# Kernel optimization log

Hardware: AMD Instinct MI355X
Metric: run time of the kernel (lower is better)

## Reference

```python
import jax, jax.numpy as jnp
import numpy as np
import math

B, T, E, H, L, FF = 8, 512, 1024, 16, 4, 4096
D = E // H
LN_EPS = 1e-5


def _layernorm(x, g, b):
    mu = jnp.mean(x, axis=-1, keepdims=True)
    var = jnp.mean((x - mu) ** 2, axis=-1, keepdims=True)
    return (x - mu) * jax.lax.rsqrt(var + LN_EPS) * g + b


def setup_inputs() -> dict:
    key = jax.random.key(0)
    ks = jax.random.split(key, 16)
    s = 0.02
    return {
        "src": jax.random.normal(ks[0], (B, T, E), jnp.float32),
        "in_proj_w": jax.random.normal(ks[1], (L, 3 * E, E), jnp.float32) * s,
        "in_proj_b": jax.random.normal(ks[2], (L, 3 * E), jnp.float32) * s,
        "out_w": jax.random.normal(ks[3], (L, E, E), jnp.float32) * s,
        "out_b": jnp.zeros((L, E), jnp.float32),
        "ff1_w": jax.random.normal(ks[4], (L, FF, E), jnp.float32) * s,
        "ff1_b": jnp.zeros((L, FF), jnp.float32),
        "ff2_w": jax.random.normal(ks[5], (L, E, FF), jnp.float32) * s,
        "ff2_b": jnp.zeros((L, E), jnp.float32),
        "ln1_g": jnp.ones((L, E), jnp.float32),
        "ln1_b": jnp.zeros((L, E), jnp.float32),
        "ln2_g": jnp.ones((L, E), jnp.float32),
        "ln2_b": jnp.zeros((L, E), jnp.float32),
        "head_w": jax.random.normal(ks[6], (1, E), jnp.float32) * s,
        "head_b": jnp.zeros((1,), jnp.float32),
    }


def reference(src, in_proj_w, in_proj_b, out_w, out_b, ff1_w, ff1_b,
              ff2_w, ff2_b, ln1_g, ln1_b, ln2_g, ln2_b, head_w, head_b):
    b, t, e = src.shape
    # --- PositionalEncoding (faithful to batch_first bug: pe indexed by batch dim) ---
    pos = jnp.arange(b, dtype=jnp.float32)[:, None]            # [B,1]
    div = jnp.exp(jnp.arange(0, e, 2, dtype=jnp.float32) * (-math.log(10000.0) / e))
    pe = jnp.zeros((b, e), jnp.float32)
    pe = pe.at[:, 0::2].set(jnp.sin(pos * div)).at[:, 1::2].set(jnp.cos(pos * div))
    x = src + pe[:, None, :]                                   # broadcast over seq

    # --- Gaussian bias, shared across layers (Tq == Tk == T) ---
    dist = jnp.arange(t)[:, None] - jnp.arange(t)[None, :]
    gb = jnp.exp(-(dist.astype(jnp.float32) ** 2) / (2.0 * (t / 4.0) ** 2))  # [T,T]

    for l in range(L):
        qkv = x @ in_proj_w[l].T + in_proj_b[l]                # [B,T,3E]
        q, k, v = jnp.split(qkv, 3, axis=-1)
        q = q.reshape(b, t, H, D).transpose(0, 2, 1, 3)        # [B,H,T,D]
        k = k.reshape(b, t, H, D).transpose(0, 2, 1, 3)
        v = v.reshape(b, t, H, D).transpose(0, 2, 1, 3)
        scores = jnp.einsum("bhqd,bhkd->bhqk", q, k) / math.sqrt(D)
        w = jax.nn.softmax(scores, axis=-1)                    # [B,H,Tq,Tk]
        w = w * gb[None, None]
        w = w / (jnp.sum(w, axis=-1, keepdims=True) + 1e-5)
        o = jnp.einsum("bhqk,bhkd->bhqd", w, v)
        o = o.transpose(0, 2, 1, 3).reshape(b, t, e)
        o = o @ out_w[l].T + out_b[l]
        x = _layernorm(x + o, ln1_g[l], ln1_b[l])              # post-norm
        ff = jax.nn.relu(x @ ff1_w[l].T + ff1_b[l]) @ ff2_w[l].T + ff2_b[l]
        x = _layernorm(x + ff, ln2_g[l], ln2_b[l])

    last = x[:, -1, :]                                         # [B,E]
    return last @ head_w.T + head_b                            # [B,1]
```

## Files before the change

kernel.cpp:

```cpp
#include <hip/hip_runtime.h>

typedef unsigned short u16;
typedef __attribute__((ext_vector_type(4))) float v4f;
typedef __attribute__((ext_vector_type(8))) short v8bf;

__device__ inline u16 f2bf(float f){
  union { float f; unsigned u; } v; v.f = f;
  unsigned r = (v.u + 0x7FFFu + ((v.u >> 16) & 1u)) >> 16;
  return (u16)r;
}
__device__ inline float bf2f(u16 u){
  union { unsigned u; float f; } v; v.u = ((unsigned)u) << 16;
  return v.f;
}

#define GLD_LDS16(gp, lp) \
  __builtin_amdgcn_global_load_lds((const __attribute__((address_space(1))) void*)(gp), \
                                   (__attribute__((address_space(3))) void*)(lp), 16, 0, 0)
#define VMCNT(n) asm volatile("s_waitcnt vmcnt(" #n ")" ::: "memory")
#define LGKM0 do { asm volatile("s_waitcnt lgkmcnt(0)" ::: "memory"); \
                   __builtin_amdgcn_sched_barrier(0); } while (0)

template<int FUSE>
__global__ __launch_bounds__(512, 2) void gemm8(
    const u16* __restrict__ A, const u16* __restrict__ W,
    const float* __restrict__ bias, void* __restrict__ C,
    int N, int K, int Kc, int gx, int gy)
{
  __shared__ u16 smem[65536];
  const int tid = threadIdx.x, lane = tid & 63, wid = tid >> 6;
  const int wm = wid >> 2, wn = wid & 3;

  const int nwg = gridDim.x, bid = blockIdx.x;
  const int swz = (bid & 7) * (nwg >> 3) + (bid >> 3);
  const int gxy = gx * gy;
  const int bz = swz / gxy;
  const int rem = swz - bz * gxy;
  const int by = rem / gx;
  const int bx = rem - by * gx;
  const int k0 = bz * Kc;
  const int NT = Kc >> 6;

  const int arow = (wid >> 1) * 16 + (lane & 15);
  const int akk  = (wid & 1) * 32 + ((lane >> 4) << 3);
  const u16* gA = A + (size_t)(by * 256 + arow) * K + k0 + akk;
  const u16* gB = W + (size_t)(bx * 256 + arow) * K + k0 + akk;
  u16* ldst = smem + tid * 8;

  auto stageA = [&](int t, int h) {
    u16* d = ldst + (t & 1) * 32768 + h * 8192;
    const u16* s = gA + (size_t)(h * 128) * K + t * 64;
    GLD_LDS16(s, d);
    GLD_LDS16(s + (size_t)64 * K, d + 4096);
  };
  auto stageB = [&](int t, int h) {
    u16* d = ldst + (t & 1) * 32768 + (2 + h) * 8192;
    const u16* s = gB + (size_t)(h * 128) * K + t * 64;
    GLD_LDS16(s, d);
    GLD_LDS16(s + (size_t)64 * K, d + 4096);
  };

  v4f acc[8][4];
  #pragma unroll
  for (int i = 0; i < 8; ++i)
    #pragma unroll
    for (int j = 0; j < 4; ++j) acc[i][j] = (v4f){0.f, 0.f, 0.f, 0.f};

  stageA(0, 0); stageB(0, 0); stageB(0, 1); stageA(0, 1);
  if (NT > 1) { stageA(1, 0); stageA(1, 1); }
  if (NT > 2) { VMCNT(4); } else { VMCNT(0); }
  __builtin_amdgcn_s_barrier();

  const u16* rdA = smem + wm * 8192 + lane * 8;
  const u16* rdB = smem + 16384 + (wn >> 1) * 8192 + lane * 8;
  const int jb = (wn & 1) * 4;

  v8bf aq[4][2], bq[2][2];

#define PHASE(QI, QJ, LOADA, LOADB, STAGE_CODE, VM_CODE)                        \
  {                                                                             \
    const int bufo = (t & 1) * 32768;                                           \
    if (LOADA) {                                                                \
      _Pragma("unroll") for (int m = 0; m < 4; ++m)                             \
        _Pragma("unroll") for (int kk = 0; kk < 2; ++kk)                        \
          aq[m][kk] = *(const v8bf*)(rdA + bufo + (((QI)*4 + m)*2 + kk)*512);   \
    }                                                                           \
    if (LOADB) {                                                                \
      _Pragma("unroll") for (int n = 0; n < 2; ++n)                             \
        _Pragma("unroll") for (int kk = 0; kk < 2; ++kk)                        \
          bq[n][kk] = *(const v8bf*)(rdB + bufo + ((jb + (QJ)*2 + n)*2 + kk)*512);\
    }                                                                           \
    STAGE_CODE;                                                                 \
    VM_CODE;                                                                    \
    __builtin_amdgcn_s_barrier();                                               \
    LGKM0;                                                                      \
    __builtin_amdgcn_s_setprio(1);                                              \
    _Pragma("unroll") for (int m = 0; m < 4; ++m)                               \
      _Pragma("unroll") for (int n = 0; n < 2; ++n)                             \
        _Pragma("unroll") for (int kk = 0; kk < 2; ++kk)                        \
          acc[(QI)*4 + m][(QJ)*2 + n] = __builtin_amdgcn_mfma_f32_16x16x32_bf16(\
              aq[m][kk], bq[n][kk], acc[(QI)*4 + m][(QJ)*2 + n], 0, 0, 0);      \
    __builtin_amdgcn_s_setprio(0);                                              \
    __builtin_amdgcn_s_barrier();                                               \
  }

  for (int t = 0; t < NT; ++t) {
    PHASE(0, 0, true,  true,
          { if (t + 1 < NT) { stageB(t + 1, 0); stageB(t + 1, 1); } }, {});
    PHASE(0, 1, false, true,  {}, {});
    PHASE(1, 1, true,  false, {}, {});
    PHASE(1, 0, false, true,
          { if (t + 2 < NT) { stageA(t + 2, 0); stageA(t + 2, 1); } },
          { if (t == NT - 2) { VMCNT(0); } else if (t < NT - 2) { VMCNT(4); } });
  }
#undef PHASE

  const int cn0 = bx * 256 + wn * 64 + (lane & 15);
  const int rm0 = by * 256 + wm * 128 + ((lane >> 4) << 2);
  if (FUSE == 2) {
    u16* Cp = (u16*)C + (size_t)bz * 4096 * N;
    #pragma unroll
    for (int i = 0; i < 8; ++i)
      #pragma unroll
      for (int r = 0; r < 4; ++r) {
        size_t ro = (size_t)(rm0 + i * 16 + r) * N + cn0;
        #pragma unroll
        for (int j = 0; j < 4; ++j) Cp[ro + j * 16] = f2bf(acc[i][j][r]);
      }
  } else {
    float bv[4];
    #pragma unroll
    for (int j = 0; j < 4; ++j) bv[j] = bias[cn0 + j * 16];
    u16* Cp = (u16*)C;
    #pragma unroll
    for (int i = 0; i < 8; ++i)
      #pragma unroll
      for (int r = 0; r < 4; ++r) {
        size_t ro = (size_t)(rm0 + i * 16 + r) * N + cn0;
        #pragma unroll
        for (int j = 0; j < 4; ++j) {
          float v = acc[i][j][r] + bv[j];
          if (FUSE == 1) v = fmaxf(v, 0.f);
          Cp[ro + j * 16] = f2bf(v);
        }
      }
  }
}

__global__ __launch_bounds__(256, 2) void attn_f(const u16* __restrict__ qkv,
                                                 u16* __restrict__ o)
{
  __shared__ u16 Kf[2][4096];
  __shared__ u16 Vt[2][4096];
  __shared__ u16 wbuf[64 * 72];
  const int tid = threadIdx.x, lane = tid & 63, wid = tid >> 6;
  const int grp = lane >> 4, li = lane & 15;
  const int bh = blockIdx.y, b = bh >> 4, h = bh & 15;
  const int q0 = blockIdx.x * 64;
  const u16* Qg = qkv + (size_t)b * 512 * 3072 + h * 64;
  const u16* Kg = Qg + 1024;
  const u16* Vg = Qg + 2048;

  const size_t qrow = (size_t)(q0 + wid * 16 + li) * 3072;
  v8bf qa0 = *(const v8bf*)(Qg + qrow + grp * 8);
  v8bf qa1 = *(const v8bf*)(Qg + qrow + 32 + grp * 8);

  const u16* kga = Kg + (size_t)(wid * 16 + li) * 3072 + grp * 8;
  auto k_stage = [&](int kt, int buf) {
    #pragma unroll
    for (int s = 0; s < 2; ++s)
      GLD_LDS16(kga + (size_t)kt * 64 * 3072 + s * 32, &Kf[buf][(wid * 2 + s) * 512]);
  };
  auto v_load = [&](int kt, int x) -> v8bf {
    int u = x * 256 + tid, kk = u >> 3, d0 = (u & 7) * 8;
    return *(const v8bf*)(Vg + (size_t)(kt * 64 + kk) * 3072 + d0);
  };
  auto vt_write = [&](int buf, int x, v8bf v) {
    int u = x * 256 + tid, kk = u >> 3, d0 = (u & 7) * 8;
    int kg = (kk >> 3) & 3, kks = kk >> 5, jb2 = (kk & 7) * 2;
    #pragma unroll
    for (int i = 0; i < 8; ++i) {
      int d = d0 + i;
      int byte = (((d >> 4) * 2 + kks) * 1024 + ((d & 15) + 16 * kg) * 16 + jb2)
                 ^ (((d >> 4) & 3) << 5);
      *(u16*)((char*)&Vt[buf][0] + byte) = (u16)v[i];
    }
  };

  v4f oacc[4];
  #pragma unroll
  for (int nt = 0; nt < 4; ++nt) oacc[nt] = (v4f){0.f, 0.f, 0.f, 0.f};
  float mreg[4] = {-1e30f, -1e30f, -1e30f, -1e30f};
  float sg[4] = {0.f, 0.f, 0.f, 0.f};
  float fqv[4];
  #pragma unroll
  for (int j = 0; j < 4; ++j) fqv[j] = (float)(q0 + wid * 16 + grp * 4 + j);

  v8bf vst[2][2];
  k_stage(0, 0);
  k_stage(1, 1);
  vst[0][0] = v_load(0, 0); vst[0][1] = v_load(0, 1);
  VMCNT(0);
  vt_write(0, 0, vst[0][0]); vt_write(0, 1, vst[0][1]);
  vst[1][0] = v_load(1, 0); vst[1][1] = v_load(1, 1);
  LGKM0;
  __builtin_amdgcn_s_barrier();

  const float GC = 3.0517578125e-05f;

  #pragma unroll
  for (int t = 0; t < 8; ++t) {
    const int cur = t & 1;
    v8bf bq0[4], bq1[4];
    #pragma unroll
    for (int nb = 0; nb < 4; ++nb) {
      bq0[nb] = *(const v8bf*)&Kf[cur][(nb * 2 + 0) * 512 + lane * 8];
      bq1[nb] = *(const v8bf*)&Kf[cur][(nb * 2 + 1) * 512 + lane * 8];
    }
    v4f pa[4];
    #pragma unroll
    for (int nb = 0; nb < 4; ++nb) {
      v4f z = (v4f){0.f, 0.f, 0.f, 0.f};
      z = __builtin_amdgcn_mfma_f32_16x16x32_bf16(qa0, bq0[nb], z, 0, 0, 0);
      pa[nb] = __builtin_amdgcn_mfma_f32_16x16x32_bf16(qa1, bq1[nb], z, 0, 0, 0);
    }
    if (t < 7) {
      __builtin_amdgcn_s_barrier();
      __builtin_amdgcn_sched_barrier(0);
      if (t + 2 < 8) k_stage(t + 2, cur);
      if (t < 6) { VMCNT(2); } else { VMCNT(0); }
      vt_write((t + 1) & 1, 0, vst[(t + 1) & 1][0]);
      vt_write((t + 1) & 1, 1, vst[(t + 1) & 1][1]);
      if (t + 2 < 8) { vst[t & 1][0] = v_load(t + 2, 0); vst[t & 1][1] = v_load(t + 2, 1); }
    }
    #pragma unroll
    for (int nb = 0; nb < 4; ++nb) {
      const float fk = (float)(t * 64 + nb * 16 + li);
      #pragma unroll
      for (int j = 0; j < 4; ++j) {
        float d = fqv[j] - fk;
        pa[nb][j] = pa[nb][j] * 0.125f - d * d * GC;
      }
    }
    #pragma unroll
    for (int j = 0; j < 4; ++j) {
      float tmax = fmaxf(fmaxf(pa[0][j], pa[1][j]), fmaxf(pa[2][j], pa[3][j]));
      tmax = fmaxf(tmax, __shfl_xor(tmax, 1));
      tmax = fmaxf(tmax, __shfl_xor(tmax, 2));
      tmax = fmaxf(tmax, __shfl_xor(tmax, 4));
      tmax = fmaxf(tmax, __shfl_xor(tmax, 8));
      float mn = fmaxf(mreg[j], tmax);
      float sc = __expf(mreg[j] - mn);
      mreg[j] = mn;
      float rs = 0.f;
      #pragma unroll
      for (int nb = 0; nb < 4; ++nb) {
        float e = __expf(pa[nb][j] - mn);
        pa[nb][j] = e;
        rs += e;
      }
      rs += __shfl_xor(rs, 1); rs += __shfl_xor(rs, 2);
      rs += __shfl_xor(rs, 4); rs += __shfl_xor(rs, 8);
      sg[j] = sg[j] * sc + rs;
      #pragma unroll
      for (int nt = 0; nt < 4; ++nt) oacc[nt][j] *= sc;
    }
    #pragma unroll
    for (int j = 0; j < 4; ++j) {
      const int row = wid * 16 + grp * 4 + j;
      #pragma unroll
      for (int nb = 0; nb < 4; ++nb)
        wbuf[row * 72 + ((nb * 16 + li) ^ (grp << 3))] = f2bf(pa[nb][j]);
    }
    const int swr = ((li >> 2) & 3) << 3;
    v8bf af0 = *(const v8bf*)&wbuf[(wid * 16 + li) * 72 + ((0 * 32 + grp * 8) ^ swr)];
    v8bf af1 = *(const v8bf*)&wbuf[(wid * 16 + li) * 72 + ((1 * 32 + grp * 8) ^ swr)];
    #pragma unroll
    for (int nt = 0; nt < 4; ++nt) {
      v8bf bv0 = *(const v8bf*)((char*)&Vt[cur][0] + ((((nt * 2 + 0) * 1024) + lane * 16) ^ ((nt & 3) << 5)));
      v8bf bv1 = *(const v8bf*)((char*)&Vt[cur][0] + ((((nt * 2 + 1) * 1024) + lane * 16) ^ ((nt & 3) << 5)));
      oacc[nt] = __builtin_amdgcn_mfma_f32_16x16x32_bf16(af0, bv0, oacc[nt], 0, 0, 0);
      oacc[nt] = __builtin_amdgcn_mfma_f32_16x16x32_bf16(af1, bv1, oacc[nt], 0, 0, 0);
    }
    if (t < 7) {
      if (t < 6) { VMCNT(2); } else { VMCNT(0); }
      LGKM0;
      __builtin_amdgcn_s_barrier();
      __builtin_amdgcn_sched_barrier(0);
    }
  }

  float rin[4];
  #pragma unroll
  for (int j = 0; j < 4; ++j) rin[j] = 1.f / sg[j];
  const size_t obase = (size_t)(b * 512 + q0 + wid * 16 + grp * 4) * 1024 + h * 64;
  #pragma unroll
  for (int nt = 0; nt < 4; ++nt)
    #pragma unroll
    for (int j = 0; j < 4; ++j)
      o[obase + (size_t)j * 1024 + nt * 16 + li] = f2bf(oacc[nt][j] * rin[j]);
}

__global__ __launch_bounds__(256) void ln_res4_k(
    const float* __restrict__ x, const u16* __restrict__ part,
    const float* __restrict__ bias, const float* __restrict__ g,
    const float* __restrict__ beta, float* __restrict__ y, u16* __restrict__ yb)
{
  const int row = blockIdx.x, tid = threadIdx.x;
  const size_t base = (size_t)row * 1024 + tid * 4;
  const size_t MN = 4096ull * 1024;
  float4 xv = *(const float4*)(x + base);
  const int e = tid * 4;
  float4 bb = *(const float4*)(bias + e);
  float v0 = xv.x + bb.x, v1 = xv.y + bb.y, v2 = xv.z + bb.z, v3 = xv.w + bb.w;
  #pragma unroll
  for (int q = 0; q < 4; ++q) {
    ushort4 pv = *(const ushort4*)(part + q * MN + base);
    v0 += bf2f(pv.x); v1 += bf2f(pv.y); v2 += bf2f(pv.z); v3 += bf2f(pv.w);
  }
  float s = v0 + v1 + v2 + v3;
  float q2 = v0*v0 + v1*v1 + v2*v2 + v3*v3;
  #pragma unroll
  for (int m = 1; m < 64; m <<= 1) { s += __shfl_xor(s, m); q2 += __shfl_xor(q2, m); }
  __shared__ float ls[4], lq[4];
  if ((tid & 63) == 0) { ls[tid >> 6] = s; lq[tid >> 6] = q2; }
  __syncthreads();
  s = ls[0] + ls[1] + ls[2] + ls[3];
  q2 = lq[0] + lq[1] + lq[2] + lq[3];
  const float mu = s * (1.f / 1024.f);
  const float var = q2 * (1.f / 1024.f) - mu * mu;
  const float rs = rsqrtf(var + 1e-5f);
  float4 gv = *(const float4*)(g + e);
  float4 be = *(const float4*)(beta + e);
  float o0 = (v0 - mu) * rs * gv.x + be.x;
  float o1 = (v1 - mu) * rs * gv.y + be.y;
  float o2 = (v2 - mu) * rs * gv.z + be.z;
  float o3 = (v3 - mu) * rs * gv.w + be.w;
  *(float4*)(y + base) = make_float4(o0, o1, o2, o3);
  ushort4 ob; ob.x = f2bf(o0); ob.y = f2bf(o1); ob.z = f2bf(o2); ob.w = f2bf(o3);
  *(ushort4*)(yb + base) = ob;
}

__global__ __launch_bounds__(256) void pe_add_k(const float* __restrict__ src,
    float* __restrict__ xf, u16* __restrict__ xb)
{
  const int idx = blockIdx.x * 256 + threadIdx.x;
  const int e = idx & 1023;
  const int b = idx >> 19;
  float freq = __expf((float)(e >> 1) * (-18.420680743952367f * (1.f / 1024.f)));
  float ang = (float)b * freq;
  float pe = (e & 1) ? cosf(ang) : sinf(ang);
  float v = src[idx] + pe;
  xf[idx] = v;
  xb[idx] = f2bf(v);
}

__global__ __launch_bounds__(256) void cvt4_k(const float* __restrict__ s0,
    const float* __restrict__ s1, const float* __restrict__ s2,
    const float* __restrict__ s3, u16* __restrict__ dst)
{
  int i = blockIdx.x * 256 + threadIdx.x;
  const float* s; size_t off;
  if (i < 786432)       { s = s0; off = (size_t)i; }
  else if (i < 1048576) { s = s1; off = (size_t)i - 786432; }
  else if (i < 2097152) { s = s2; off = (size_t)i - 1048576; }
  else                  { s = s3; off = (size_t)i - 2097152; }
  float4 v = ((const float4*)s)[off];
  ushort4 ov; ov.x = f2bf(v.x); ov.y = f2bf(v.y); ov.z = f2bf(v.z); ov.w = f2bf(v.w);
  ((ushort4*)dst)[i] = ov;
}

__global__ __launch_bounds__(256) void head_k(const float* __restrict__ xf,
    const float* __restrict__ hw, const float* __restrict__ hb, float* __restrict__ out)
{
  const int b = blockIdx.x, tid = threadIdx.x;
  const float4 xv = ((const float4*)(xf + ((size_t)b * 512 + 511) * 1024))[tid];
  const float4 wv = ((const float4*)hw)[tid];
  float s = xv.x * wv.x + xv.y * wv.y + xv.z * wv.z + xv.w * wv.w;
  #pragma unroll
  for (int m = 1; m < 64; m <<= 1) s += __shfl_xor(s, m);
  __shared__ float ls[4];
  if ((tid & 63) == 0) ls[tid >> 6] = s;
  __syncthreads();
  if (tid == 0) out[b] = ls[0] + ls[1] + ls[2] + ls[3] + hb[0];
}

extern "C" void kernel_launch(void* const* d_in, const int* in_sizes, int n_in,
                              void* d_out, int out_size, void* d_ws, size_t ws_size,
                              hipStream_t stream)
{
  const float* src  = (const float*)d_in[0];
  const float* ipw  = (const float*)d_in[1];
  const float* ipb  = (const float*)d_in[2];
  const float* outw = (const float*)d_in[3];
  const float* outb = (const float*)d_in[4];
  const float* f1w  = (const float*)d_in[5];
  const float* f1b  = (const float*)d_in[6];
  const float* f2w  = (const float*)d_in[7];
  const float* f2b  = (const float*)d_in[8];
  const float* l1g  = (const float*)d_in[9];
  const float* l1b  = (const float*)d_in[10];
  const float* l2g  = (const float*)d_in[11];
  const float* l2b  = (const float*)d_in[12];
  const float* hw   = (const float*)d_in[13];
  const float* hb   = (const float*)d_in[14];

  char* p = (char*)d_ws;
  auto take = [&](size_t bytes) { char* r = p; p += (bytes + 255) & ~(size_t)255; return r; };
  float* xf   = (float*)take(4096ull * 1024 * 4);
  u16*   xb   = (u16*)  take(4096ull * 1024 * 2);
  u16*   slA  = (u16*)  take(4096ull * 4096 * 2);
  u16*   ob   = (u16*)  take(4096ull * 1024 * 2);
  u16*   pf   = (u16*)  take(4ull * 4096 * 1024 * 2);
  u16*   wc   = (u16*)  take(12582912ull * 2);

  u16* qkvb = slA;
  u16* f1o  = slA;

  pe_add_k<<<16384, 256, 0, stream>>>(src, xf, xb);

  for (int l = 0; l < 4; ++l) {
    cvt4_k<<<12288, 256, 0, stream>>>(ipw + (size_t)l * 3145728,
                                      outw + (size_t)l * 1048576,
                                      f1w + (size_t)l * 4194304,
                                      f2w + (size_t)l * 4194304, wc);
    gemm8<0><<<192, 512, 0, stream>>>(xb, wc, ipb + l * 3072, qkvb, 3072, 1024, 1024, 12, 16);
    attn_f<<<dim3(8, 128), 256, 0, stream>>>(qkvb, ob);
    gemm8<2><<<256, 512, 0, stream>>>(ob, wc + 3145728, nullptr, pf, 1024, 1024, 256, 4, 16);
    ln_res4_k<<<4096, 256, 0, stream>>>(xf, pf, outb + l * 1024, l1g + l * 1024, l1b + l * 1024, xf, xb);
    gemm8<1><<<256, 512, 0, stream>>>(xb, wc + 4194304, f1b + l * 4096, f1o, 4096, 1024, 1024, 16, 16);
    gemm8<2><<<256, 512, 0, stream>>>(f1o, wc + 8388608, nullptr, pf, 1024, 4096, 1024, 4, 16);
    ln_res4_k<<<4096, 256, 0, stream>>>(xf, pf, f2b + l * 1024, l2g + l * 1024, l2b + l * 1024, xf, xb);
  }
  head_k<<<8, 256, 0, stream>>>(xf, hw, hb, (float*)d_out);
}
```

Before: 910.8 us.

## Replace 256x256 double-buffered GEMM with 128x256 triple-buffered K=32 pipeline

Shrinks the GEMM output tile from 256x256 to 128x256 and the K step from 64 to 32, with a three-stage LDS ring buffer and one barrier per step instead of the four-phase schedule. LDS per block and accumulator registers drop, so launch bounds now request 4 blocks per CU, and the grids double to give more workgroups. The aim is more latency hiding and better CU fill. The cost is lower arithmetic intensity per tile, more A/B reloads from global memory, and more barriers per unit of compute.

New measurement: 1.032 ms. 13.3% more time.

```diff
diff --git a/kernel.cpp b/kernel.cpp
--- a/kernel.cpp
+++ b/kernel.cpp
@@ -22,12 +22,12 @@
                    __builtin_amdgcn_sched_barrier(0); } while (0)
 
 template<int FUSE>
-__global__ __launch_bounds__(512, 2) void gemm8(
+__global__ __launch_bounds__(512, 4) void gemm3(
     const u16* __restrict__ A, const u16* __restrict__ W,
     const float* __restrict__ bias, void* __restrict__ C,
     int N, int K, int Kc, int gx, int gy)
 {
-  __shared__ u16 smem[65536];
+  __shared__ u16 smem[36864];
   const int tid = threadIdx.x, lane = tid & 63, wid = tid >> 6;
   const int wm = wid >> 2, wn = wid & 3;
 
@@ -38,110 +38,84 @@
   const int rem = swz - bz * gxy;
   const int by = rem / gx;
   const int bx = rem - by * gx;
+  const int m0 = by * 128, n0 = bx * 256;
   const int k0 = bz * Kc;
-  const int NT = Kc >> 6;
-
-  const int arow = (wid >> 1) * 16 + (lane & 15);
-  const int akk  = (wid & 1) * 32 + ((lane >> 4) << 3);
-  const u16* gA = A + (size_t)(by * 256 + arow) * K + k0 + akk;
-  const u16* gB = W + (size_t)(bx * 256 + arow) * K + k0 + akk;
+  const int NT = Kc >> 5;
+
+  const int l15 = lane & 15, kc8 = (lane >> 4) * 8;
+  const u16* srcA  = A + (size_t)(m0 + wid * 16 + l15) * K + k0 + kc8;
+  const u16* srcB0 = W + (size_t)(n0 + wid * 16 + l15) * K + k0 + kc8;
+  const u16* srcB1 = W + (size_t)(n0 + 128 + wid * 16 + l15) * K + k0 + kc8;
   u16* ldst = smem + tid * 8;
 
-  auto stageA = [&](int t, int h) {
-    u16* d = ldst + (t & 1) * 32768 + h * 8192;
-    const u16* s = gA + (size_t)(h * 128) * K + t * 64;
-    GLD_LDS16(s, d);
-    GLD_LDS16(s + (size_t)64 * K, d + 4096);
+  auto stage = [&](int t) {
+    u16* d = ldst + (t % 3) * 12288;
+    const int ko = t * 32;
+    GLD_LDS16(srcA  + ko, d);
+    GLD_LDS16(srcB0 + ko, d + 4096);
+    GLD_LDS16(srcB1 + ko, d + 8192);
   };
-  auto stageB = [&](int t, int h) {
-    u16* d = ldst + (t & 1) * 32768 + (2 + h) * 8192;
-    const u16* s = gB + (size_t)(h * 128) * K + t * 64;
-    GLD_LDS16(s, d);
-    GLD_LDS16(s + (size_t)64 * K, d + 4096);
-  };
-
-  v4f acc[8][4];
-  #pragma unroll
-  for (int i = 0; i < 8; ++i)
-    #pragma unroll
-    for (int j = 0; j < 4; ++j) acc[i][j] = (v4f){0.f, 0.f, 0.f, 0.f};
-
-  stageA(0, 0); stageB(0, 0); stageB(0, 1); stageA(0, 1);
-  if (NT > 1) { stageA(1, 0); stageA(1, 1); }
-  if (NT > 2) { VMCNT(4); } else { VMCNT(0); }
+
+  v4f acc[4][4];
+  #pragma unroll
+  for (int m = 0; m < 4; ++m)
+    #pragma unroll
+    for (int n = 0; n < 4; ++n) acc[m][n] = (v4f){0.f, 0.f, 0.f, 0.f};
+
+  stage(0); stage(1);
+  VMCNT(3);
   __builtin_amdgcn_s_barrier();
 
-  const u16* rdA = smem + wm * 8192 + lane * 8;
-  const u16* rdB = smem + 16384 + (wn >> 1) * 8192 + lane * 8;
-  const int jb = (wn & 1) * 4;
-
-  v8bf aq[4][2], bq[2][2];
-
-#define PHASE(QI, QJ, LOADA, LOADB, STAGE_CODE, VM_CODE)                        \
-  {                                                                             \
-    const int bufo = (t & 1) * 32768;                                           \
-    if (LOADA) {                                                                \
-      _Pragma("unroll") for (int m = 0; m < 4; ++m)                             \
-        _Pragma("unroll") for (int kk = 0; kk < 2; ++kk)                        \
-          aq[m][kk] = *(const v8bf*)(rdA + bufo + (((QI)*4 + m)*2 + kk)*512);   \
-    }                                                                           \
-    if (LOADB) {                                                                \
-      _Pragma("unroll") for (int n = 0; n < 2; ++n)                             \
-        _Pragma("unroll") for (int kk = 0; kk < 2; ++kk)                        \
-          bq[n][kk] = *(const v8bf*)(rdB + bufo + ((jb + (QJ)*2 + n)*2 + kk)*512);\
-    }                                                                           \
-    STAGE_CODE;                                                                 \
-    VM_CODE;                                                                    \
-    __builtin_amdgcn_s_barrier();                                               \
-    LGKM0;                                                                      \
-    __builtin_amdgcn_s_setprio(1);                                              \
-    _Pragma("unroll") for (int m = 0; m < 4; ++m)                               \
-      _Pragma("unroll") for (int n = 0; n < 2; ++n)                             \
-        _Pragma("unroll") for (int kk = 0; kk < 2; ++kk)                        \
-          acc[(QI)*4 + m][(QJ)*2 + n] = __builtin_amdgcn_mfma_f32_16x16x32_bf16(\
-              aq[m][kk], bq[n][kk], acc[(QI)*4 + m][(QJ)*2 + n], 0, 0, 0);      \
-    __builtin_amdgcn_s_setprio(0);                                              \
-    __builtin_amdgcn_s_barrier();                                               \
+  const u16* rdA = smem + (wm * 4) * 512 + lane * 8;
+  const u16* rdB = smem + 4096 + (wn * 4) * 512 + lane * 8;
+
+  for (int t = 0; t < NT; ++t) {
+    const int bo = (t % 3) * 12288;
+    v8bf aq[4], bq[4];
+    #pragma unroll
+    for (int m = 0; m < 4; ++m) aq[m] = *(const v8bf*)(rdA + bo + m * 512);
+    #pragma unroll
+    for (int n = 0; n < 4; ++n) bq[n] = *(const v8bf*)(rdB + bo + n * 512);
+    if (t + 2 < NT) stage(t + 2);
+    LGKM0;
+    __builtin_amdgcn_s_setprio(1);
+    #pragma unroll
+    for (int m = 0; m < 4; ++m)
+      #pragma unroll
+      for (int n = 0; n < 4; ++n)
+        acc[m][n] = __builtin_amdgcn_mfma_f32_16x16x32_bf16(aq[m], bq[n], acc[m][n], 0, 0, 0);
+    __builtin_amdgcn_s_setprio(0);
+    if (t < NT - 2) { VMCNT(3); } else if (t == NT - 2) { VMCNT(0); }
+    __builtin_amdgcn_s_barrier();
   }
 
-  for (int t = 0; t < NT; ++t) {
-    PHASE(0, 0, true,  true,
-          { if (t + 1 < NT) { stageB(t + 1, 0); stageB(t + 1, 1); } }, {});
-    PHASE(0, 1, false, true,  {}, {});
-    PHASE(1, 1, true,  false, {}, {});
-    PHASE(1, 0, false, true,
-          { if (t + 2 < NT) { stageA(t + 2, 0); stageA(t + 2, 1); } },
-          { if (t == NT - 2) { VMCNT(0); } else if (t < NT - 2) { VMCNT(4); } });
-  }
-#undef PHASE
-
-  const int cn0 = bx * 256 + wn * 64 + (lane & 15);
-  const int rm0 = by * 256 + wm * 128 + ((lane >> 4) << 2);
+  const int cn0 = n0 + wn * 64 + l15;
+  const int rm0 = m0 + wm * 64 + ((lane >> 4) << 2);
   if (FUSE == 2) {
     u16* Cp = (u16*)C + (size_t)bz * 4096 * N;
     #pragma unroll
-    for (int i = 0; i < 8; ++i)
+    for (int m = 0; m < 4; ++m)
       #pragma unroll
       for (int r = 0; r < 4; ++r) {
-        size_t ro = (size_t)(rm0 + i * 16 + r) * N + cn0;
+        size_t ro = (size_t)(rm0 + m * 16 + r) * N + cn0;
         #pragma unroll
-        for (int j = 0; j < 4; ++j) Cp[ro + j * 16] = f2bf(acc[i][j][r]);
+        for (int n = 0; n < 4; ++n) Cp[ro + n * 16] = f2bf(acc[m][n][r]);
       }
   } else {
     float bv[4];
     #pragma unroll
-    for (int j = 0; j < 4; ++j) bv[j] = bias[cn0 + j * 16];
+    for (int n = 0; n < 4; ++n) bv[n] = bias[cn0 + n * 16];
     u16* Cp = (u16*)C;
     #pragma unroll
-    for (int i = 0; i < 8; ++i)
+    for (int m = 0; m < 4; ++m)
       #pragma unroll
       for (int r = 0; r < 4; ++r) {
-        size_t ro = (size_t)(rm0 + i * 16 + r) * N + cn0;
+        size_t ro = (size_t)(rm0 + m * 16 + r) * N + cn0;
         #pragma unroll
-        for (int j = 0; j < 4; ++j) {
-          float v = acc[i][j][r] + bv[j];
+        for (int n = 0; n < 4; ++n) {
+          float v = acc[m][n][r] + bv[n];
           if (FUSE == 1) v = fmaxf(v, 0.f);
-          Cp[ro + j * 16] = f2bf(v);
+          Cp[ro + n * 16] = f2bf(v);
         }
       }
   }
@@ -424,12 +398,12 @@
                                       outw + (size_t)l * 1048576,
                                       f1w + (size_t)l * 4194304,
                                       f2w + (size_t)l * 4194304, wc);
-    gemm8<0><<<192, 512, 0, stream>>>(xb, wc, ipb + l * 3072, qkvb, 3072, 1024, 1024, 12, 16);
+    gemm3<0><<<384, 512, 0, stream>>>(xb, wc, ipb + l * 3072, qkvb, 3072, 1024, 1024, 12, 32);
     attn_f<<<dim3(8, 128), 256, 0, stream>>>(qkvb, ob);
-    gemm8<2><<<256, 512, 0, stream>>>(ob, wc + 3145728, nullptr, pf, 1024, 1024, 256, 4, 16);
+    gemm3<2><<<512, 512, 0, stream>>>(ob, wc + 3145728, nullptr, pf, 1024, 1024, 256, 4, 32);
     ln_res4_k<<<4096, 256, 0, stream>>>(xf, pf, outb + l * 1024, l1g + l * 1024, l1b + l * 1024, xf, xb);
-    gemm8<1><<<256, 512, 0, stream>>>(xb, wc + 4194304, f1b + l * 4096, f1o, 4096, 1024, 1024, 16, 16);
-    gemm8<2><<<256, 512, 0, stream>>>(f1o, wc + 8388608, nullptr, pf, 1024, 4096, 1024, 4, 16);
+    gemm3<1><<<512, 512, 0, stream>>>(xb, wc + 4194304, f1b + l * 4096, f1o, 4096, 1024, 1024, 16, 32);
+    gemm3<2><<<512, 512, 0, stream>>>(f1o, wc + 8388608, nullptr, pf, 1024, 4096, 1024, 4, 32);
     ln_res4_k<<<4096, 256, 0, stream>>>(xf, pf, f2b + l * 1024, l2g + l * 1024, l2b + l * 1024, xf, xb);
   }
   head_k<<<8, 256, 0, stream>>>(xf, hw, hb, (float*)d_out);
```
